# Kernel tuning notes

Hardware: AMD Instinct MI355X
Metric: run time of the kernel (lower is better)

The kernel has to match this reference:

```python
import jax, jax.numpy as jnp
import numpy as np

ALPHABET = 4
SKETCH_DIM = 128
SUBSEQ = 8
SEQ_LEN = 8192


def setup_inputs() -> dict:
    key = jax.random.key(0)
    k1, k2, k3 = jax.random.split(key, 3)
    sequence = jax.random.randint(k1, (SEQ_LEN,), 0, ALPHABET, dtype=jnp.int32)
    # stacked Linear(A, d, bias=False) weights, xavier-uniform-ish init
    limit = float(np.sqrt(6.0 / (ALPHABET + SKETCH_DIM)))
    hash_weights = jax.random.uniform(k2, (SUBSEQ, SKETCH_DIM, ALPHABET),
                                      minval=-limit, maxval=limit, dtype=jnp.float32)
    sign_weights = jax.random.normal(k3, (SUBSEQ, ALPHABET), dtype=jnp.float32)
    return {"sequence": sequence, "hash_weights": hash_weights, "sign_weights": sign_weights}


def _sketch(sequence, hash_weights, sign_weights):
    P, d, A = hash_weights.shape
    seq_len = sequence.shape[0]
    # circulant gather indices: roll(src, s)[j] == src[(j - s) % d]
    j = jnp.arange(d)
    idx = (j[:, None] - j[None, :]) % d  # [d(out), d(shift)]
    p_ids = jnp.arange(1, P + 1)
    z_num = p_ids.astype(jnp.float32)

    Tp0 = jnp.zeros((P + 1, d), jnp.float32).at[0, 0].set(1.0)
    Tm0 = jnp.zeros((P + 1, d), jnp.float32)

    def step(carry, xs):
        Tp, Tm = carry
        i, c = xs
        valid = (c >= 0) & (c < A)
        cc = jnp.clip(c, 0, A - 1)
        hv = hash_weights[:, :, cc]                      # [P, d]
        probs = jax.nn.softmax(hv, axis=1)               # [P, d]
        sign = jax.nn.sigmoid(sign_weights[:, cc])       # [P]
        denom = (i + 1).astype(jnp.float32)
        z = (z_num / denom)[:, None]                     # [P, 1]
        gate = ((p_ids <= i + 1) & valid)[:, None]       # [P, 1]
        # soft circular shift: sum_s probs[s] * roll(source, s)
        convP = jnp.einsum('pjs,ps->pj', Tp[:P][:, idx], probs)
        convM = jnp.einsum('pjs,ps->pj', Tm[:P][:, idx], probs)
        newP = jnp.where(gate, (1.0 - z) * Tp[1:] + z * sign[:, None] * convP, Tp[1:])
        newM = jnp.where(gate, (1.0 - z) * Tm[1:] + z * (1.0 - sign[:, None]) * convM, Tm[1:])
        return (Tp.at[1:].set(newP), Tm.at[1:].set(newM)), None

    (Tp, Tm), _ = jax.lax.scan(step, (Tp0, Tm0), (jnp.arange(seq_len), sequence))
    return Tp[P] - Tm[P]


def reference(sequence, hash_weights, sign_weights):
    return _sketch(sequence, hash_weights, sign_weights)
```

## Files before the change

kernel.cpp:

```cpp
#include <hip/hip_runtime.h>
#include <math.h>

#define DDIM 128
#define NSEQ 8192
#define SUB 16
#define SEG 64
#define NSEGB 128
#define NTRI 45

#define TRI(L,q) ((L)*((L)+1)/2 + (q))

#define OFF_PHAT 0
#define OFF_AB   32768
#define OFF_MSEG 557056
#define OFF_MT1  6455296
#define OFF_MT2  7929856

__device__ __forceinline__ void loadG(const float2* __restrict__ p, int fq,
                                      float (&R)[NTRI], float (&I)[NTRI]) {
#pragma unroll
  for (int e = 0; e < NTRI; ++e) {
    float2 t = p[e*128 + fq];
    R[e] = t.x; I[e] = t.y;
  }
}

__device__ __forceinline__ void publish(float2* __restrict__ b, int fq,
                                        const float (&R)[NTRI], const float (&I)[NTRI]) {
#pragma unroll
  for (int e = 0; e < NTRI; ++e) b[e*128 + fq] = make_float2(R[e], I[e]);
}

__device__ __forceinline__ void matvec(const float (&GR)[NTRI], const float (&GI)[NTRI],
                                       float (&vr)[9], float (&vi)[9]) {
#pragma unroll
  for (int L = 8; L >= 0; --L) {
    float sr = 0.f, si = 0.f;
#pragma unroll
    for (int q = 0; q <= L; ++q) {
      float xr = vr[q], xi = vi[q];
      sr += GR[TRI(L,q)]*xr - GI[TRI(L,q)]*xi;
      si += GR[TRI(L,q)]*xi + GI[TRI(L,q)]*xr;
    }
    vr[L] = sr; vi[L] = si;
  }
}

__device__ __forceinline__ void matmulL(const float2* __restrict__ b, int fq,
                                        float (&Ar)[NTRI], float (&Ai)[NTRI]) {
#pragma unroll
  for (int L = 8; L >= 0; --L) {
    float Br_[9], Bi_[9];
#pragma unroll
    for (int r = 0; r <= L; ++r) {
      float2 t = b[TRI(L,r)*128 + fq];
      Br_[r] = t.x; Bi_[r] = t.y;
    }
    float tr[9], ti[9];
#pragma unroll
    for (int q = 0; q <= L; ++q) {
      float sr = 0.f, si = 0.f;
#pragma unroll
      for (int r = q; r <= L; ++r) {
        float ar = Ar[TRI(r,q)], ai = Ai[TRI(r,q)];
        sr += Br_[r]*ar - Bi_[r]*ai;
        si += Br_[r]*ai + Bi_[r]*ar;
      }
      tr[q] = sr; ti[q] = si;
    }
#pragma unroll
    for (int q = 0; q <= L; ++q) { Ar[TRI(L,q)] = tr[q]; Ai[TRI(L,q)] = ti[q]; }
  }
}

__global__ __launch_bounds__(128)
void sk_setup(const int* __restrict__ seq,
              const float* __restrict__ hw,
              const float* __restrict__ sw,
              float2* __restrict__ phat,
              float2* __restrict__ ab)
{
  const int tid = threadIdx.x;
  const int bid = blockIdx.x;

  if (bid < 32) {
    __shared__ float probs[128];
    __shared__ float ct[128], st[128];
    __shared__ float red[4];
    const int r = bid, p = r >> 2, c = r & 3;
    const int wave = tid >> 6, lane = tid & 63;

    float h = hw[p*512 + tid*4 + c];
    float mx = h;
    #pragma unroll
    for (int off = 1; off < 64; off <<= 1) mx = fmaxf(mx, __shfl_xor(mx, off));
    if (lane == 0) red[wave] = mx;
    __syncthreads();
    mx = fmaxf(red[0], red[1]);
    float e = expf(h - mx);
    float s = e;
    #pragma unroll
    for (int off = 1; off < 64; off <<= 1) s += __shfl_xor(s, off);
    if (lane == 0) red[2 + wave] = s;
    float th = 6.28318530717958647692f * (float)tid / 128.0f;
    ct[tid] = cosf(th); st[tid] = sinf(th);
    __syncthreads();
    s = red[2] + red[3];
    probs[tid] = e / s;
    __syncthreads();

    float ar = 0.f, ai = 0.f;
    for (int j = 0; j < 128; ++j) {
      float pv = probs[j];
      int w = (j * tid) & 127;
      ar += pv * ct[w];
      ai -= pv * st[w];
    }
    phat[(c*8 + p)*128 + tid] = make_float2(ar, ai);
  } else {
    const int total = NSEQ * 8;
    for (int n = (bid - 32)*128 + tid; n < total; n += 64*128) {
      const int i = n >> 3, Lm1 = n & 7, L = Lm1 + 1;
      int cc0 = seq[i];
      bool valid = (cc0 >= 0) && (cc0 < 4);
      int cc = min(max(cc0, 0), 3);
      bool gate = valid && (L <= i + 1);
      float z  = (float)L / (float)(i + 1);
      float sg = 1.0f / (1.0f + expf(-sw[Lm1*4 + cc]));
      float a = gate ? (1.0f - z) : 1.0f;
      float b = gate ? (z * sg) : 0.0f;
      ab[n] = make_float2(a, b);
    }
  }
}

__global__ __launch_bounds__(512)
void sk_seg(const int* __restrict__ seq,
            const float2* __restrict__ phat_g,
            const float2* __restrict__ ab_g,
            float2* __restrict__ mseg)
{
  __shared__ float2 phS[4096];
  __shared__ float2 abS[SEG*8];
  __shared__ int    chS[SEG];
  __shared__ float2 tb[2][NTRI*128];
  const int tid = threadIdx.x;
  const int u   = tid >> 7, fq = tid & 127;
  const int m   = blockIdx.x;

  {
    const float4* src = (const float4*)phat_g;
    float4* dst = (float4*)phS;
    for (int i = tid; i < 2048; i += 512) dst[i] = src[i];
  }
  for (int i = tid; i < SEG*8; i += 512) abS[i] = ab_g[m*SEG*8 + i];
  if (tid < SEG) chS[tid] = seq[m*SEG + tid];
  __syncthreads();

  float Mr[NTRI], Mi[NTRI];
  #pragma unroll
  for (int e = 0; e < NTRI; ++e) { Mr[e] = 0.f; Mi[e] = 0.f; }
  #pragma unroll
  for (int L = 0; L <= 8; ++L) Mr[TRI(L,L)] = 1.0f;

  const int t0 = u * SUB;
  for (int t = 0; t < SUB; ++t) {
    const int ts = t0 + t;
    const int c  = chS[ts];
    #pragma unroll
    for (int L = 8; L >= 1; --L) {
      float2 abv = abS[ts*8 + (L-1)];
      float2 Pv  = phS[(c*8 + (L-1))*128 + fq];
      const float a = abv.x;
      const float bPr = abv.y * Pv.x, bPi = abv.y * Pv.y;
      #pragma unroll
      for (int q = 0; q < L; ++q) {
        float xr = Mr[TRI(L-1,q)], xi = Mi[TRI(L-1,q)];
        Mr[TRI(L,q)] = a*Mr[TRI(L,q)] + (bPr*xr - bPi*xi);
        Mi[TRI(L,q)] = a*Mi[TRI(L,q)] + (bPr*xi + bPi*xr);
      }
      Mr[TRI(L,L)] *= a;
      Mi[TRI(L,L)] *= a;
    }
  }

  if (u == 1 || u == 3) publish(tb[u >> 1], fq, Mr, Mi);
  __syncthreads();
  if (u == 0 || u == 2) matmulL(tb[u >> 1], fq, Mr, Mi);
  __syncthreads();
  if (u == 2) publish(tb[1], fq, Mr, Mi);
  __syncthreads();
  if (u == 0) {
    matmulL(tb[1], fq, Mr, Mi);
    #pragma unroll
    for (int e = 0; e < NTRI; ++e)
      mseg[((size_t)m*NTRI + e)*128 + fq] = make_float2(Mr[e], Mi[e]);
  }
}

__global__ __launch_bounds__(512)
void sk_comb(const float2* __restrict__ min_, float2* __restrict__ mout)
{
  __shared__ float2 tb[2][NTRI*128];
  const int tid = threadIdx.x;
  const int u   = tid >> 7, fq = tid & 127;
  const int g   = blockIdx.x;

  float Ar[NTRI], Ai[NTRI];
  loadG(min_ + (size_t)(g*4 + u) * NTRI * 128, fq, Ar, Ai);

  if (u == 1 || u == 3) publish(tb[u >> 1], fq, Ar, Ai);
  __syncthreads();
  if (u == 0 || u == 2) matmulL(tb[u >> 1], fq, Ar, Ai);
  __syncthreads();
  if (u == 2) publish(tb[1], fq, Ar, Ai);
  __syncthreads();
  if (u == 0) {
    matmulL(tb[1], fq, Ar, Ai);
    #pragma unroll
    for (int e = 0; e < NTRI; ++e)
      mout[((size_t)g*NTRI + e)*128 + fq] = make_float2(Ar[e], Ai[e]);
  }
}

__global__ __launch_bounds__(512)
void sk_fin8(const float2* __restrict__ mg, float* __restrict__ out)
{
  __shared__ float2 tb[2][NTRI*128];
  __shared__ float2 vS[9*128];
  __shared__ float Ur[128], Ui[128], ct[128], st[128];
  const int tid = threadIdx.x;
  const int u   = tid >> 7, fq = tid & 127;

  float Ar[NTRI], Ai[NTRI];
  loadG(mg + (size_t)u * NTRI * 128, fq, Ar, Ai);

  if (tid < 128) {
    float th = 6.28318530717958647692f * (float)tid / 128.0f;
    ct[tid] = cosf(th); st[tid] = sinf(th);
  }

  if (u == 1 || u == 3) publish(tb[u >> 1], fq, Ar, Ai);
  __syncthreads();
  if (u == 0 || u == 2) matmulL(tb[u >> 1], fq, Ar, Ai);
  __syncthreads();
  if (u == 2) publish(tb[1], fq, Ar, Ai);
  __syncthreads();
  if (u == 0) {
    matmulL(tb[1], fq, Ar, Ai);
    #pragma unroll
    for (int L = 0; L <= 8; ++L)
      vS[L*128 + fq] = make_float2(Ar[TRI(L,0)], Ai[TRI(L,0)]);
  }
  __syncthreads();

  loadG(mg + (size_t)(4 + u) * NTRI * 128, fq, Ar, Ai);
  if (u == 1 || u == 3) publish(tb[u >> 1], fq, Ar, Ai);
  __syncthreads();
  if (u == 0 || u == 2) matmulL(tb[u >> 1], fq, Ar, Ai);
  __syncthreads();
  if (u == 2) publish(tb[1], fq, Ar, Ai);
  __syncthreads();
  if (u == 0) {
    matmulL(tb[1], fq, Ar, Ai);
    float vr[9], vi[9];
    #pragma unroll
    for (int L = 0; L <= 8; ++L) { float2 t = vS[L*128 + fq]; vr[L] = t.x; vi[L] = t.y; }
    matvec(Ar, Ai, vr, vi);
    Ur[fq] = vr[8]; Ui[fq] = vi[8];
  }
  __syncthreads();

  if (tid < 128) {
    float acc = 0.f;
    for (int k = 0; k < 128; ++k) {
      int w = (tid * k) & 127;
      acc += Ur[k]*ct[w] - Ui[k]*st[w];
    }
    out[tid] = acc * (1.0f/128.0f);
  }
}

extern "C" void kernel_launch(void* const* d_in, const int* in_sizes, int n_in,
                              void* d_out, int out_size, void* d_ws, size_t ws_size,
                              hipStream_t stream)
{
  const int*   seq = (const int*)d_in[0];
  const float* hw  = (const float*)d_in[1];
  const float* sw  = (const float*)d_in[2];

  char* base = (char*)d_ws;
  float2* phat = (float2*)(base + OFF_PHAT);
  float2* ab   = (float2*)(base + OFF_AB);
  float2* mseg = (float2*)(base + OFF_MSEG);
  float2* mt1  = (float2*)(base + OFF_MT1);
  float2* mt2  = (float2*)(base + OFF_MT2);

  sk_setup<<<96, 128, 0, stream>>>(seq, hw, sw, phat, ab);
  sk_seg<<<NSEGB, 512, 0, stream>>>(seq, phat, ab, mseg);
  sk_comb<<<32, 512, 0, stream>>>(mseg, mt1);
  sk_comb<<<8, 512, 0, stream>>>(mt1, mt2);
  sk_fin8<<<1, 512, 0, stream>>>(mt2, (float*)d_out);
}
```

Baseline: 124.0 us.

## Fuse gate coefficient computation into segment kernel and merge combine levels

```diff
diff --git a/kernel.cpp b/kernel.cpp
--- a/kernel.cpp
+++ b/kernel.cpp
@@ -11,10 +11,8 @@
 #define TRI(L,q) ((L)*((L)+1)/2 + (q))
 
 #define OFF_PHAT 0
-#define OFF_AB   32768
-#define OFF_MSEG 557056
-#define OFF_MT1  6455296
-#define OFF_MT2  7929856
+#define OFF_MSEG 32768
+#define OFF_MT2  5931008
 
 __device__ __forceinline__ void loadG(const float2* __restrict__ p, int fq,
                                       float (&R)[NTRI], float (&I)[NTRI]) {
@@ -46,7 +44,7 @@
   }
 }
 
-__device__ __forceinline__ void matmulL(const float2* __restrict__ b, int fq,
+__device__ __forceinline__ void matmulS(const float2* __restrict__ b, int fq,
                                         float (&Ar)[NTRI], float (&Ai)[NTRI]) {
 #pragma unroll
   for (int L = 8; L >= 0; --L) {
@@ -74,70 +72,49 @@
 }
 
 __global__ __launch_bounds__(128)
-void sk_setup(const int* __restrict__ seq,
-              const float* __restrict__ hw,
-              const float* __restrict__ sw,
-              float2* __restrict__ phat,
-              float2* __restrict__ ab)
-{
-  const int tid = threadIdx.x;
-  const int bid = blockIdx.x;
-
-  if (bid < 32) {
-    __shared__ float probs[128];
-    __shared__ float ct[128], st[128];
-    __shared__ float red[4];
-    const int r = bid, p = r >> 2, c = r & 3;
-    const int wave = tid >> 6, lane = tid & 63;
-
-    float h = hw[p*512 + tid*4 + c];
-    float mx = h;
-    #pragma unroll
-    for (int off = 1; off < 64; off <<= 1) mx = fmaxf(mx, __shfl_xor(mx, off));
-    if (lane == 0) red[wave] = mx;
-    __syncthreads();
-    mx = fmaxf(red[0], red[1]);
-    float e = expf(h - mx);
-    float s = e;
-    #pragma unroll
-    for (int off = 1; off < 64; off <<= 1) s += __shfl_xor(s, off);
-    if (lane == 0) red[2 + wave] = s;
-    float th = 6.28318530717958647692f * (float)tid / 128.0f;
-    ct[tid] = cosf(th); st[tid] = sinf(th);
-    __syncthreads();
-    s = red[2] + red[3];
-    probs[tid] = e / s;
-    __syncthreads();
-
-    float ar = 0.f, ai = 0.f;
-    for (int j = 0; j < 128; ++j) {
-      float pv = probs[j];
-      int w = (j * tid) & 127;
-      ar += pv * ct[w];
-      ai -= pv * st[w];
-    }
-    phat[(c*8 + p)*128 + tid] = make_float2(ar, ai);
-  } else {
-    const int total = NSEQ * 8;
-    for (int n = (bid - 32)*128 + tid; n < total; n += 64*128) {
-      const int i = n >> 3, Lm1 = n & 7, L = Lm1 + 1;
-      int cc0 = seq[i];
-      bool valid = (cc0 >= 0) && (cc0 < 4);
-      int cc = min(max(cc0, 0), 3);
-      bool gate = valid && (L <= i + 1);
-      float z  = (float)L / (float)(i + 1);
-      float sg = 1.0f / (1.0f + expf(-sw[Lm1*4 + cc]));
-      float a = gate ? (1.0f - z) : 1.0f;
-      float b = gate ? (z * sg) : 0.0f;
-      ab[n] = make_float2(a, b);
-    }
-  }
+void sk_phat(const float* __restrict__ hw,
+             float2* __restrict__ phat)
+{
+  __shared__ float probs[128];
+  __shared__ float ct[128], st[128];
+  __shared__ float red[4];
+  const int tid = threadIdx.x;
+  const int r = blockIdx.x, p = r >> 2, c = r & 3;
+  const int wave = tid >> 6, lane = tid & 63;
+
+  float h = hw[p*512 + tid*4 + c];
+  float mx = h;
+  #pragma unroll
+  for (int off = 1; off < 64; off <<= 1) mx = fmaxf(mx, __shfl_xor(mx, off));
+  if (lane == 0) red[wave] = mx;
+  __syncthreads();
+  mx = fmaxf(red[0], red[1]);
+  float e = expf(h - mx);
+  float s = e;
+  #pragma unroll
+  for (int off = 1; off < 64; off <<= 1) s += __shfl_xor(s, off);
+  if (lane == 0) red[2 + wave] = s;
+  float th = 6.28318530717958647692f * (float)tid / 128.0f;
+  ct[tid] = cosf(th); st[tid] = sinf(th);
+  __syncthreads();
+  s = red[2] + red[3];
+  probs[tid] = e / s;
+  __syncthreads();
+
+  float ar = 0.f, ai = 0.f;
+  for (int j = 0; j < 128; ++j) {
+    float pv = probs[j];
+    int w = (j * tid) & 127;
+    ar += pv * ct[w];
+    ai -= pv * st[w];
+  }
+  phat[(c*8 + p)*128 + tid] = make_float2(ar, ai);
 }
 
 __global__ __launch_bounds__(512)
 void sk_seg(const int* __restrict__ seq,
+            const float* __restrict__ sw,
             const float2* __restrict__ phat_g,
-            const float2* __restrict__ ab_g,
             float2* __restrict__ mseg)
 {
   __shared__ float2 phS[4096];
@@ -153,8 +130,18 @@
     float4* dst = (float4*)phS;
     for (int i = tid; i < 2048; i += 512) dst[i] = src[i];
   }
-  for (int i = tid; i < SEG*8; i += 512) abS[i] = ab_g[m*SEG*8 + i];
   if (tid < SEG) chS[tid] = seq[m*SEG + tid];
+  {
+    const int ts = tid >> 3, Lm1 = tid & 7, L = Lm1 + 1;
+    const int i = m*SEG + ts;
+    int c0 = seq[i];
+    bool valid = (c0 >= 0) && (c0 < 4);
+    int cc = min(max(c0, 0), 3);
+    bool gate = valid && (L <= i + 1);
+    float z  = (float)L / (float)(i + 1);
+    float sg = 1.0f / (1.0f + expf(-sw[Lm1*4 + cc]));
+    abS[tid] = make_float2(gate ? (1.0f - z) : 1.0f, gate ? (z * sg) : 0.0f);
+  }
   __syncthreads();
 
   float Mr[NTRI], Mi[NTRI];
@@ -186,12 +173,12 @@
 
   if (u == 1 || u == 3) publish(tb[u >> 1], fq, Mr, Mi);
   __syncthreads();
-  if (u == 0 || u == 2) matmulL(tb[u >> 1], fq, Mr, Mi);
+  if (u == 0 || u == 2) matmulS(tb[u >> 1], fq, Mr, Mi);
   __syncthreads();
   if (u == 2) publish(tb[1], fq, Mr, Mi);
   __syncthreads();
   if (u == 0) {
-    matmulL(tb[1], fq, Mr, Mi);
+    matmulS(tb[1], fq, Mr, Mi);
     #pragma unroll
     for (int e = 0; e < NTRI; ++e)
       mseg[((size_t)m*NTRI + e)*128 + fq] = make_float2(Mr[e], Mi[e]);
@@ -199,24 +186,28 @@
 }
 
 __global__ __launch_bounds__(512)
-void sk_comb(const float2* __restrict__ min_, float2* __restrict__ mout)
+void sk_comb16(const float2* __restrict__ min_, float2* __restrict__ mout)
 {
   __shared__ float2 tb[2][NTRI*128];
   const int tid = threadIdx.x;
   const int u   = tid >> 7, fq = tid & 127;
   const int g   = blockIdx.x;
+  const float2* bp = min_ + (size_t)(g*16 + u*4) * NTRI * 128;
 
   float Ar[NTRI], Ai[NTRI];
-  loadG(min_ + (size_t)(g*4 + u) * NTRI * 128, fq, Ar, Ai);
+  loadG(bp, fq, Ar, Ai);
+  matmulS(bp + (size_t)1*NTRI*128, fq, Ar, Ai);
+  matmulS(bp + (size_t)2*NTRI*128, fq, Ar, Ai);
+  matmulS(bp + (size_t)3*NTRI*128, fq, Ar, Ai);
 
   if (u == 1 || u == 3) publish(tb[u >> 1], fq, Ar, Ai);
   __syncthreads();
-  if (u == 0 || u == 2) matmulL(tb[u >> 1], fq, Ar, Ai);
+  if (u == 0 || u == 2) matmulS(tb[u >> 1], fq, Ar, Ai);
   __syncthreads();
   if (u == 2) publish(tb[1], fq, Ar, Ai);
   __syncthreads();
   if (u == 0) {
-    matmulL(tb[1], fq, Ar, Ai);
+    matmulS(tb[1], fq, Ar, Ai);
     #pragma unroll
     for (int e = 0; e < NTRI; ++e)
       mout[((size_t)g*NTRI + e)*128 + fq] = make_float2(Ar[e], Ai[e]);
@@ -242,12 +233,12 @@
 
   if (u == 1 || u == 3) publish(tb[u >> 1], fq, Ar, Ai);
   __syncthreads();
-  if (u == 0 || u == 2) matmulL(tb[u >> 1], fq, Ar, Ai);
+  if (u == 0 || u == 2) matmulS(tb[u >> 1], fq, Ar, Ai);
   __syncthreads();
   if (u == 2) publish(tb[1], fq, Ar, Ai);
   __syncthreads();
   if (u == 0) {
-    matmulL(tb[1], fq, Ar, Ai);
+    matmulS(tb[1], fq, Ar, Ai);
     #pragma unroll
     for (int L = 0; L <= 8; ++L)
       vS[L*128 + fq] = make_float2(Ar[TRI(L,0)], Ai[TRI(L,0)]);
@@ -257,12 +248,12 @@
   loadG(mg + (size_t)(4 + u) * NTRI * 128, fq, Ar, Ai);
   if (u == 1 || u == 3) publish(tb[u >> 1], fq, Ar, Ai);
   __syncthreads();
-  if (u == 0 || u == 2) matmulL(tb[u >> 1], fq, Ar, Ai);
+  if (u == 0 || u == 2) matmulS(tb[u >> 1], fq, Ar, Ai);
   __syncthreads();
   if (u == 2) publish(tb[1], fq, Ar, Ai);
   __syncthreads();
   if (u == 0) {
-    matmulL(tb[1], fq, Ar, Ai);
+    matmulS(tb[1], fq, Ar, Ai);
     float vr[9], vi[9];
     #pragma unroll
     for (int L = 0; L <= 8; ++L) { float2 t = vS[L*128 + fq]; vr[L] = t.x; vi[L] = t.y; }
@@ -291,14 +282,11 @@
 
   char* base = (char*)d_ws;
   float2* phat = (float2*)(base + OFF_PHAT);
-  float2* ab   = (float2*)(base + OFF_AB);
   float2* mseg = (float2*)(base + OFF_MSEG);
-  float2* mt1  = (float2*)(base + OFF_MT1);
   float2* mt2  = (float2*)(base + OFF_MT2);
 
-  sk_setup<<<96, 128, 0, stream>>>(seq, hw, sw, phat, ab);
-  sk_seg<<<NSEGB, 512, 0, stream>>>(seq, phat, ab, mseg);
-  sk_comb<<<32, 512, 0, stream>>>(mseg, mt1);
-  sk_comb<<<8, 512, 0, stream>>>(mt1, mt2);
+  sk_phat<<<32, 128, 0, stream>>>(hw, phat);
+  sk_seg<<<NSEGB, 512, 0, stream>>>(seq, sw, phat, mseg);
+  sk_comb16<<<8, 512, 0, stream>>>(mseg, mt2);
   sk_fin8<<<1, 512, 0, stream>>>(mt2, (float*)d_out);
 }
```

Measured after the change: 159.4 us. 1.29x slower.
